# Optimization experiments

Measured on AMD Instinct MI355X. Metric: run time of the kernel, lower is better.

## Reference

```python
import jax, jax.numpy as jnp
import numpy as np
from jax.scipy.linalg import solve_triangular

N, S, G, D = 2048, 64, 1, 512


def setup_inputs() -> dict:
    key = jax.random.key(0)
    k1, k2, k3, k4 = jax.random.split(key, 4)
    x = jax.random.normal(k1, (N, D), jnp.float32)
    mu = jax.random.uniform(k2, (S, G, D), jnp.float32) - 0.5  # torch.rand(...) - 0.5
    omega = jax.random.normal(k3, (S, G), jnp.float32)
    # original init sets sigma_p = eye; perturb so m = A^T A has distinct eigenvalues
    sigma_p = jnp.eye(D, dtype=jnp.float32)[None, None] + 0.05 * jax.random.normal(k4, (S, G, D, D), jnp.float32)
    return {"x": x, "mu": mu, "omega": omega, "sigma_p": sigma_p}


def reference(x, mu, omega, sigma_p):
    d = x.shape[-1]
    # m = sigma_p^T @ sigma_p  (symmetric PSD), per class/component
    m = jnp.einsum('sgki,sgkj->sgij', sigma_p, sigma_p)  # (S,G,D,D)
    # torch: sigma = m + 0.01 * diag_embed(eig(m).eigenvalues.real) * eye(d)
    # m is symmetric PSD -> eigenvalues are real; eigvalsh is the batched symmetric form
    eigvals = jnp.linalg.eigvalsh(m)  # (S,G,D)
    sigma = m + 0.01 * eigvals[..., None] * jnp.eye(d, dtype=m.dtype)  # adds diag(eigvals)
    _ = jax.nn.softmax(omega, -1)  # computed in original forward but unused in output
    mu0 = mu[:, 0]        # (S,D)   only component 0 is used
    sig0 = sigma[:, 0]    # (S,D,D)
    # MultivariateNormal.log_prob via Cholesky, batched over classes and samples
    L = jnp.linalg.cholesky(sig0)               # (S,D,D)
    diff = x[None, :, :] - mu0[:, None, :]      # (S,N,D)
    z = solve_triangular(L, diff.swapaxes(-1, -2), lower=True)  # (S,D,N)
    maha = jnp.sum(z * z, axis=1)               # (S,N)
    logdet = 2.0 * jnp.sum(jnp.log(jnp.diagonal(L, axis1=-2, axis2=-1)), axis=-1)  # (S,)
    logp = -0.5 * (maha + logdet[:, None] + d * jnp.log(jnp.asarray(2.0 * np.pi, m.dtype)))
    return logp.T  # (N,S)
```

## Files before the change

### kernel.cpp

```cpp
#include <hip/hip_runtime.h>

#define D 512
#define TW 16

__device__ __forceinline__ float waveSum(float v) {
#pragma unroll
    for (int m = 32; m > 0; m >>= 1) v += __shfl_xor(v, m, 64);
    return v;
}
__device__ __forceinline__ float waveMin(float v) {
#pragma unroll
    for (int m = 32; m > 0; m >>= 1) v = fminf(v, __shfl_xor(v, m, 64));
    return v;
}
__device__ __forceinline__ float waveMax(float v) {
#pragma unroll
    for (int m = 32; m > 0; m >>= 1) v = fmaxf(v, __shfl_xor(v, m, 64));
    return v;
}

__global__ __launch_bounds__(256) void xpose_kernel(const float* __restrict__ x,
                                                    float* __restrict__ xT) {
    __shared__ float t[64][65];
    const int bx = blockIdx.x * 64;
    const int by = blockIdx.y * 64;
    const int tid = threadIdx.x;
    const int lx = tid & 63, lq = tid >> 6;
#pragma unroll
    for (int r = 0; r < 64; r += 4)
        t[r + lq][lx] = x[(size_t)(bx + r + lq) * D + by + lx];
    __syncthreads();
#pragma unroll
    for (int r = 0; r < 64; r += 4)
        xT[(size_t)(by + r + lq) * 2048 + bx + lx] = t[lx][r + lq];
}

__global__ __launch_bounds__(256) void syrk_kernel(const float* __restrict__ sp,
                                                   float* __restrict__ M) {
    const int s = blockIdx.y;
    const int I = blockIdx.x >> 3, J = blockIdx.x & 7;
    const int tx = threadIdx.x & 15, ty = threadIdx.x >> 4;
    const float* __restrict__ A = sp + (size_t)s * D * D;
    __shared__ __align__(16) float As[64 * 68];
    __shared__ __align__(16) float Bs[64 * 68];
    float acc[4][4];
#pragma unroll
    for (int r = 0; r < 4; r++)
#pragma unroll
        for (int q = 0; q < 4; q++) acc[r][q] = 0.f;

    for (int k0 = 0; k0 < D; k0 += 64) {
        for (int e = threadIdx.x; e < 4096; e += 256) {
            const int col = e & 63, kr = e >> 6;
            As[kr * 68 + col] = A[(size_t)(k0 + kr) * D + I * 64 + col];
            Bs[kr * 68 + col] = A[(size_t)(k0 + kr) * D + J * 64 + col];
        }
        __syncthreads();
#pragma unroll 4
        for (int k = 0; k < 64; k++) {
            const float4 a = *(const float4*)&As[k * 68 + 4 * ty];
            const float4 b = *(const float4*)&Bs[k * 68 + 4 * tx];
            const float av[4] = {a.x, a.y, a.z, a.w};
            const float bv[4] = {b.x, b.y, b.z, b.w};
#pragma unroll
            for (int r = 0; r < 4; r++)
#pragma unroll
                for (int q = 0; q < 4; q++) acc[r][q] += av[r] * bv[q];
        }
        __syncthreads();
    }
#pragma unroll
    for (int r = 0; r < 4; r++) {
        float4 v4;
        v4.x = acc[r][0]; v4.y = acc[r][1]; v4.z = acc[r][2]; v4.w = acc[r][3];
        const size_t off = (size_t)s * D * D + (size_t)(I * 64 + 4 * ty + r) * D + J * 64 + 4 * tx;
        *(float4*)(M + off) = v4;
    }
}

__global__ __launch_bounds__(1024) void latrd_panel(float* __restrict__ T,
                                                    float* __restrict__ Vt,
                                                    float* __restrict__ Wt,
                                                    float* __restrict__ dvec,
                                                    float* __restrict__ evec,
                                                    int ps, int jmax) {
    const int s = blockIdx.x;
    float* __restrict__ Ts = T + (size_t)s * D * D;
    float* __restrict__ Vg = Vt + (size_t)s * 32 * D;
    float* __restrict__ Wg = Wt + (size_t)s * 32 * D;
    const int tid = threadIdx.x, lane = tid & 63, wid = tid >> 6;
    const int l4 = lane & 15, quad = lane >> 4;
    extern __shared__ float sm[];
    float* __restrict__ Vs = sm;
    float* __restrict__ Ws = sm + 16896;
    float* __restrict__ vb = sm + 33792;
    float* __restrict__ pf = sm + 34304;
    float* __restrict__ c1 = sm + 34816;
    float* __restrict__ c2 = sm + 34848;
    float* __restrict__ red = sm + 34880;
    float* __restrict__ sca = sm + 34896;

    for (int i = tid; i < 34304; i += 1024) sm[i] = 0.f;
    __syncthreads();

    float rk = (tid < D) ? Ts[(size_t)ps * D + tid] : 0.f;

    for (int j = 0; j < jmax; j++) {
        const int k = ps + j, sup = k + 1;
        float val = 0.f;
        if (tid < D && tid > k) {
            float corr = 0.f;
#pragma unroll 4
            for (int t = 0; t < j; t++)
                corr += Vs[tid * 33 + t] * Ws[k * 33 + t]
                      + Ws[tid * 33 + t] * Vs[k * 33 + t];
            val = rk - corr;
            vb[tid] = val;
            if (tid == sup) sca[3] = val;
        } else if (tid == k) {
            float dc = 0.f;
            for (int t = 0; t < j; t++) dc += Vs[k * 33 + t] * Ws[k * 33 + t];
            dvec[s * D + k] = rk - 2.f * dc;
            vb[k] = 0.f;
        }
        float xp = (tid < D && tid > sup) ? val * val : 0.f;
        xp = waveSum(xp);
        if (lane == 0) red[wid] = xp;
        __syncthreads();

        float xn2 = 0.f;
#pragma unroll
        for (int q = 0; q < TW; q++) xn2 += red[q];
        const float a0 = sca[3];
        const int skip = (xn2 <= 0.f);
        float beta = 0.f, v0 = 0.f, alpha = a0;
        if (!skip) {
            const float an = sqrtf(a0 * a0 + xn2);
            alpha = (a0 >= 0.f) ? -an : an;
            v0 = a0 - alpha;
            beta = 2.f / (v0 * v0 + xn2);
        }
        if (tid == sup) {
            evec[s * D + k] = skip ? a0 : alpha;
            if (!skip) vb[sup] = v0;
        }
        if (!skip) {
            const int t = tid >> 5, r = tid & 31;
            float a1 = 0.f, a2 = 0.f;
            for (int i = sup + 1 + r; i < D; i += 32) {
                const float v = vb[i];
                a1 += Ws[i * 33 + t] * v;
                a2 += Vs[i * 33 + t] * v;
            }
#pragma unroll
            for (int m = 16; m > 0; m >>= 1) {
                a1 += __shfl_xor(a1, m, 64);
                a2 += __shfl_xor(a2, m, 64);
            }
            if (r == 0) {
                c1[t] = a1 + Ws[sup * 33 + t] * v0;
                c2[t] = a2 + Vs[sup * 33 + t] * v0;
            }
        }
        __syncthreads();
        if (skip) {
            if (tid < D && tid >= sup) { Vg[j * D + tid] = 0.f; Wg[j * D + tid] = 0.f; }
            if (tid < D && k + 1 < D) rk = Ts[(size_t)(k + 1) * D + tid];
            __syncthreads();
            continue;
        }

        const int w0 = sup & ~63;
        float pvw = 0.f;
        for (int i = sup + (wid * 4 + quad); i < D; i += 64) {
            const float* __restrict__ row = Ts + (size_t)i * D;
            float4 a4 = {0.f, 0.f, 0.f, 0.f};
            for (int c = w0 + 4 * l4; c < D; c += 64) {
                const float4 a = *(const float4*)&row[c];
                const float4 b = *(const float4*)&vb[c];
                a4.x += a.x * b.x; a4.y += a.y * b.y;
                a4.z += a.z * b.z; a4.w += a.w * b.w;
            }
            float t1 = (a4.x + a4.y) + (a4.z + a4.w);
            t1 -= Vs[i * 33 + l4] * c1[l4] + Vs[i * 33 + l4 + 16] * c1[l4 + 16]
                + Ws[i * 33 + l4] * c2[l4] + Ws[i * 33 + l4 + 16] * c2[l4 + 16];
#pragma unroll
            for (int m = 1; m < 16; m <<= 1) t1 += __shfl_xor(t1, m, 64);
            const float p = beta * t1;
            if (l4 == 0) pf[i] = p;
            pvw += p * vb[i];
        }
        pvw += __shfl_xor(pvw, 16, 64);
        pvw += __shfl_xor(pvw, 32, 64);
        if (lane == 0) red[wid] = pvw;
        __syncthreads();

        float pv = 0.f;
#pragma unroll
        for (int q = 0; q < TW; q++) pv += red[q];
        const float cc = 0.5f * beta * pv;
        if (tid < D) {
            if (tid >= sup) {
                const float v = vb[tid];
                const float w = pf[tid] - cc * v;
                Vs[tid * 33 + j] = v;
                Ws[tid * 33 + j] = w;
                Vg[j * D + tid] = v;
                Wg[j * D + tid] = w;
            }
            if (k + 1 < D) rk = Ts[(size_t)(k + 1) * D + tid];
        }
        __syncthreads();
    }
    if (ps + jmax == D - 2 && tid == 0) {
        const int k1 = D - 2, k2 = D - 1;
        float dc = 0.f, ec = 0.f, dc2 = 0.f;
        for (int t = 0; t < jmax; t++) {
            dc  += Vs[k1 * 33 + t] * Ws[k1 * 33 + t];
            ec  += Vs[k1 * 33 + t] * Ws[k2 * 33 + t]
                 + Ws[k1 * 33 + t] * Vs[k2 * 33 + t];
            dc2 += Vs[k2 * 33 + t] * Ws[k2 * 33 + t];
        }
        dvec[s * D + k1] = Ts[(size_t)k1 * D + k1] - 2.f * dc;
        evec[s * D + k1] = Ts[(size_t)k1 * D + k2] - ec;
        dvec[s * D + k2] = Ts[(size_t)k2 * D + k2] - 2.f * dc2;
        evec[s * D + k2] = 0.f;
    }
}

__global__ __launch_bounds__(256) void latrd_update(float* __restrict__ T,
                                                    const float* __restrict__ Vt,
                                                    const float* __restrict__ Wt,
                                                    int r0) {
    const int s = blockIdx.z;
    const int i0 = r0 + 64 * blockIdx.y;
    const int j0 = r0 + 64 * blockIdx.x;
    float* __restrict__ Ts = T + (size_t)s * D * D;
    const float* __restrict__ Vg = Vt + (size_t)s * 32 * D;
    const float* __restrict__ Wg = Wt + (size_t)s * 32 * D;
    __shared__ __align__(16) float Vi[32 * 68], Wi[32 * 68], Vj[32 * 68], Wj[32 * 68];
    const int tid = threadIdx.x, tx = tid & 15, ty = tid >> 4;
    const float4 z4 = {0.f, 0.f, 0.f, 0.f};
    for (int e = tid; e < 512; e += 256) {
        const int t = e >> 4, c4 = (e & 15) * 4;
        const int gi = i0 + c4, gj = j0 + c4;
        *(float4*)&Vi[t * 68 + c4] = (gi < D) ? *(const float4*)&Vg[t * D + gi] : z4;
        *(float4*)&Wi[t * 68 + c4] = (gi < D) ? *(const float4*)&Wg[t * D + gi] : z4;
        *(float4*)&Vj[t * 68 + c4] = (gj < D) ? *(const float4*)&Vg[t * D + gj] : z4;
        *(float4*)&Wj[t * 68 + c4] = (gj < D) ? *(const float4*)&Wg[t * D + gj] : z4;
    }
    __syncthreads();
    float acc[4][4] = {{0.f}};
#pragma unroll 4
    for (int t = 0; t < 32; t++) {
        const float4 va = *(const float4*)&Vi[t * 68 + 4 * ty];
        const float4 wa = *(const float4*)&Wi[t * 68 + 4 * ty];
        const float4 vc = *(const float4*)&Vj[t * 68 + 4 * tx];
        const float4 wc = *(const float4*)&Wj[t * 68 + 4 * tx];
        const float av[4] = {va.x, va.y, va.z, va.w};
        const float aw[4] = {wa.x, wa.y, wa.z, wa.w};
        const float bv[4] = {vc.x, vc.y, vc.z, vc.w};
        const float bw[4] = {wc.x, wc.y, wc.z, wc.w};
#pragma unroll
        for (int r = 0; r < 4; r++)
#pragma unroll
            for (int q = 0; q < 4; q++) acc[r][q] += av[r] * bw[q] + aw[r] * bv[q];
    }
    const int gj = j0 + 4 * tx;
    if (gj >= D) return;
#pragma unroll
    for (int r = 0; r < 4; r++) {
        const int gi = i0 + 4 * ty + r;
        if (gi >= D) continue;
        float4 c = *(float4*)&Ts[(size_t)gi * D + gj];
        c.x -= acc[r][0]; c.y -= acc[r][1]; c.z -= acc[r][2]; c.w -= acc[r][3];
        *(float4*)&Ts[(size_t)gi * D + gj] = c;
    }
}

__global__ __launch_bounds__(512) void bisect_kernel(const float* __restrict__ dvec,
                                                     const float* __restrict__ evec,
                                                     float* __restrict__ lam) {
    const int s = blockIdx.x, tid = threadIdx.x;
    const int lane = tid & 63, wid = tid >> 6;
    __shared__ float d[D], e2[D], ea[D];
    __shared__ float red[8];
    __shared__ float sh_lo, sh_hi;
    {
        const float dv = dvec[s * D + tid];
        const float ev = evec[s * D + tid];
        d[tid] = dv; ea[tid] = fabsf(ev); e2[tid] = ev * ev;
    }
    __syncthreads();
    const float rad = ea[tid] + ((tid > 0) ? ea[tid - 1] : 0.f);
    float lo = waveMin(d[tid] - rad);
    float hi = waveMax(d[tid] + rad);
    if (lane == 0) red[wid] = lo;
    __syncthreads();
    if (tid == 0) {
        float t = red[0];
        for (int q = 1; q < 8; q++) t = fminf(t, red[q]);
        sh_lo = t - 1e-3f * fmaxf(fabsf(t), 1.f);
    }
    __syncthreads();
    if (lane == 0) red[wid] = hi;
    __syncthreads();
    if (tid == 0) {
        float t = red[0];
        for (int q = 1; q < 8; q++) t = fmaxf(t, red[q]);
        sh_hi = t + 1e-3f * fmaxf(fabsf(t), 1.f);
    }
    __syncthreads();
    float a = sh_lo, b = sh_hi;
    const int j1 = tid + 1;
    for (int it = 0; it < 36; it++) {
        const float mid = 0.5f * (a + b);
        int cnt = 0;
        float q = d[0] - mid;
        cnt += (q < 0.f);
        for (int i = 1; i < D; i++) {
            float den = q;
            const float ad = fabsf(den);
            den = (ad < 1e-26f) ? ((den < 0.f) ? -1e-26f : 1e-26f) : den;
            q = d[i] - mid - e2[i - 1] / den;
            cnt += (q < 0.f);
        }
        if (cnt >= j1) b = mid; else a = mid;
    }
    lam[s * D + tid] = 0.5f * (a + b);
}

__global__ __launch_bounds__(256) void chol_panel(float* __restrict__ M,
                                                  const float* __restrict__ lam,
                                                  float* __restrict__ logdet,
                                                  float* __restrict__ Lp,
                                                  int j0, int first) {
    const int s = blockIdx.x;
    float* __restrict__ Ms = M + (size_t)s * D * D;
    float* __restrict__ Lps = Lp + (size_t)s * 32 * D;
    const int tid = threadIdx.x, lane = tid & 63, wid = tid >> 6;
    extern __shared__ float smc[];
    float* __restrict__ P = smc;
    const int Wd = D - j0;
    for (int e = tid; e < 32 * D; e += 256) {
        const int t = e >> 9, i = e & 511;
        if (i >= j0) {
            const int il = i - j0;
            float v = Ms[(size_t)(j0 + t) * D + i];
            if (il == t) v += 0.01f * lam[s * D + j0 + t];
            P[t * 520 + il] = v;
        }
    }
    __syncthreads();
    float lacc = 0.f;
    for (int jl = 0; jl < 32; jl++) {
        const float pd = P[jl * 520 + jl];
        const float inv = 1.f / sqrtf(pd);
        if (tid == 0) { lacc += 0.5f * logf(pd); P[jl * 520 + jl] = sqrtf(pd); }
        for (int il = jl + 1 + tid; il < Wd; il += 256) P[jl * 520 + il] *= inv;
        __syncthreads();
        for (int kk = jl + 1 + wid; kk < 32; kk += 4) {
            const float f = P[jl * 520 + kk];
            for (int il = kk + lane; il < Wd; il += 64) P[kk * 520 + il] -= f * P[jl * 520 + il];
        }
        __syncthreads();
    }
    if (tid == 0) logdet[s] = (first ? 0.f : logdet[s]) + 2.f * lacc;
    for (int e = tid; e < 32 * D; e += 256) {
        const int t = e >> 9, i = e & 511;
        const int il = i - j0;
        if (il >= t) Ms[(size_t)(j0 + t) * D + i] = P[t * 520 + il];
        if (i >= j0 + 32) Lps[(size_t)t * D + i] = P[t * 520 + il];
    }
}

__global__ __launch_bounds__(256) void chol_update(float* __restrict__ M,
                                                   const float* __restrict__ Lp,
                                                   int r0) {
    if (blockIdx.x < blockIdx.y) return;
    const int s = blockIdx.z;
    const int i0 = r0 + 64 * blockIdx.y;
    const int j0 = r0 + 64 * blockIdx.x;
    float* __restrict__ Ms = M + (size_t)s * D * D;
    const float* __restrict__ Lps = Lp + (size_t)s * 32 * D;
    __shared__ __align__(16) float Li[32 * 68], Lj[32 * 68];
    const int tid = threadIdx.x, tx = tid & 15, ty = tid >> 4;
    const float4 z4 = {0.f, 0.f, 0.f, 0.f};
    for (int e = tid; e < 512; e += 256) {
        const int t = e >> 4, c4 = (e & 15) * 4;
        const int gi = i0 + c4, gj = j0 + c4;
        *(float4*)&Li[t * 68 + c4] = (gi < D) ? *(const float4*)&Lps[(size_t)t * D + gi] : z4;
        *(float4*)&Lj[t * 68 + c4] = (gj < D) ? *(const float4*)&Lps[(size_t)t * D + gj] : z4;
    }
    __syncthreads();
    float acc[4][4] = {{0.f}};
#pragma unroll 4
    for (int t = 0; t < 32; t++) {
        const float4 a = *(const float4*)&Li[t * 68 + 4 * ty];
        const float4 b = *(const float4*)&Lj[t * 68 + 4 * tx];
        const float av[4] = {a.x, a.y, a.z, a.w};
        const float bv[4] = {b.x, b.y, b.z, b.w};
#pragma unroll
        for (int r = 0; r < 4; r++)
#pragma unroll
            for (int q = 0; q < 4; q++) acc[r][q] += av[r] * bv[q];
    }
    const int gj = j0 + 4 * tx;
    if (gj >= D) return;
#pragma unroll
    for (int r = 0; r < 4; r++) {
        const int gi = i0 + 4 * ty + r;
        if (gi >= D) continue;
        float4 c = *(float4*)&Ms[(size_t)gi * D + gj];
        c.x -= acc[r][0]; c.y -= acc[r][1]; c.z -= acc[r][2]; c.w -= acc[r][3];
        *(float4*)&Ms[(size_t)gi * D + gj] = c;
    }
}

__global__ __launch_bounds__(64) void invdiag_kernel(const float* __restrict__ M,
                                                     float* __restrict__ invDT) {
    const int b = blockIdx.x, s = b >> 3, I = b & 7;
    const int c = threadIdx.x;
    __shared__ float Lsh[64 * 65];
    __shared__ float xsh[64 * 65];
    const float* __restrict__ Ms = M + (size_t)s * D * D;
    for (int e = c; e < 4096; e += 64) {
        const int i = e & 63, k = e >> 6;
        Lsh[i * 65 + k] = Ms[(size_t)(I * 64 + k) * D + I * 64 + i];
    }
    for (int i = 0; i < 64; i++) xsh[c * 65 + i] = (i == c) ? 1.f : 0.f;
    __syncthreads();
    for (int i = 0; i < 64; i++) {
        float t = xsh[c * 65 + i];
        for (int k = 0; k < i; k++) t -= Lsh[i * 65 + k] * xsh[c * 65 + k];
        xsh[c * 65 + i] = t / Lsh[i * 65 + i];
    }
    float* __restrict__ outp = invDT + (size_t)b * 4096 + c * 64;
    for (int i = 0; i < 64; i++) outp[i] = xsh[c * 65 + i];
}

__global__ __launch_bounds__(256) void trsm_kernel(const float* __restrict__ M,
                                                   const float* __restrict__ invDT,
                                                   const float* __restrict__ xT,
                                                   const float* __restrict__ mu,
                                                   const float* __restrict__ logdet,
                                                   float* __restrict__ out) {
    extern __shared__ float smem[];
    float* __restrict__ Z = smem;
    float* __restrict__ U = smem + 512 * 33;
    const int s = blockIdx.y;
    const int n0 = blockIdx.x * 32;
    const int tid = threadIdx.x;
    const int tx = tid & 15, ty = tid >> 4;
    const float* __restrict__ Ms = M + (size_t)s * D * D;
    const float* __restrict__ mus = mu + s * D;

    for (int I = 0; I < 8; I++) {
        float acc[4][2];
#pragma unroll
        for (int r = 0; r < 4; r++) {
            const int irow = I * 64 + 4 * ty + r;
            const float m0 = mus[irow];
            const float2 xv = *(const float2*)&xT[(size_t)irow * 2048 + n0 + 2 * tx];
            acc[r][0] = xv.x - m0;
            acc[r][1] = xv.y - m0;
        }
        for (int J = 0; J < I; J++) {
#pragma unroll
            for (int h = 0; h < 2; h++) {
                __syncthreads();
                for (int e = tid; e < 512; e += 256) {
                    const int i4 = (e & 15) * 4, kk = e >> 4;
                    *(float4*)&U[kk * 68 + i4] =
                        *(const float4*)&Ms[(size_t)(J * 64 + 32 * h + kk) * D + I * 64 + i4];
                }
                __syncthreads();
#pragma unroll 8
                for (int kk = 0; kk < 32; kk++) {
                    const float4 a = *(const float4*)&U[kk * 68 + 4 * ty];
                    const float2 b = *(const float2*)&Z[(J * 64 + 32 * h + kk) * 33 + 2 * tx];
                    const float av[4] = {a.x, a.y, a.z, a.w};
#pragma unroll
                    for (int r = 0; r < 4; r++) {
                        acc[r][0] -= av[r] * b.x;
                        acc[r][1] -= av[r] * b.y;
                    }
                }
            }
        }
        __syncthreads();
#pragma unroll
        for (int r = 0; r < 4; r++) {
            float2 v2; v2.x = acc[r][0]; v2.y = acc[r][1];
            *(float2*)&U[(4 * ty + r) * 34 + 2 * tx] = v2;
        }
        __syncthreads();
        {
            float z[4][2] = {{0.f}};
            const float* __restrict__ iD = invDT + (size_t)(s * 8 + I) * 4096;
#pragma unroll 8
            for (int kk = 0; kk < 64; kk++) {
                const float4 a = *(const float4*)&iD[kk * 64 + 4 * ty];
                const float2 b = *(const float2*)&U[kk * 34 + 2 * tx];
                const float av[4] = {a.x, a.y, a.z, a.w};
#pragma unroll
                for (int r = 0; r < 4; r++) {
                    z[r][0] += av[r] * b.x;
                    z[r][1] += av[r] * b.y;
                }
            }
#pragma unroll
            for (int r = 0; r < 4; r++) {
                float2 v2; v2.x = z[r][0]; v2.y = z[r][1];
                *(float2*)&Z[(I * 64 + 4 * ty + r) * 33 + 2 * tx] = v2;
            }
        }
    }
    __syncthreads();
    {
        const int c = tid & 31, part = tid >> 5;
        float sum = 0.f;
        for (int i = part * 64; i < part * 64 + 64; i++) {
            const float z = Z[i * 33 + c];
            sum += z * z;
        }
        U[part * 32 + c] = sum;
    }
    __syncthreads();
    if (tid < 32) {
        float mah = 0.f;
#pragma unroll
        for (int p = 0; p < 8; p++) mah += U[p * 32 + tid];
        out[(size_t)(n0 + tid) * 64 + s] = -0.5f * (mah + logdet[s] + 940.993058f);
    }
}

extern "C" void kernel_launch(void* const* d_in, const int* in_sizes, int n_in,
                              void* d_out, int out_size, void* d_ws, size_t ws_size,
                              hipStream_t stream) {
    const float* x  = (const float*)d_in[0];
    const float* mu = (const float*)d_in[1];
    const float* sp = (const float*)d_in[3];
    float* out = (float*)d_out;

    float* wsf  = (float*)d_ws;
    float* MT   = wsf;
    float* dvec = wsf + (size_t)16777216;
    float* evec = dvec + 32768;
    float* lamv = evec + 32768;
    float* logd = lamv + 32768;
    float* Vt   = logd + 64;
    float* Wt   = Vt + (size_t)1048576;
    float* xT   = Wt + (size_t)1048576;
    float* Lp   = Vt;
    float* invDT = Vt;

    xpose_kernel<<<dim3(32, 8), dim3(256), 0, stream>>>(x, xT);
    syrk_kernel<<<dim3(64, 64), dim3(256), 0, stream>>>(sp, MT);

    const size_t plds = (size_t)34900 * sizeof(float);
    for (int p = 0; p < 16; p++) {
        const int ps = 32 * p;
        const int jmax = (p == 15) ? 30 : 32;
        latrd_panel<<<dim3(64), dim3(1024), plds, stream>>>(MT, Vt, Wt, dvec, evec, ps, jmax);
        if (p < 15) {
            const int r0 = ps + 32;
            const int nt = (D - r0 + 63) / 64;
            latrd_update<<<dim3(nt, nt, 64), dim3(256), 0, stream>>>(MT, Vt, Wt, r0);
        }
    }

    bisect_kernel<<<dim3(64), dim3(512), 0, stream>>>(dvec, evec, lamv);

    syrk_kernel<<<dim3(64, 64), dim3(256), 0, stream>>>(sp, MT);
    const size_t clds = (size_t)(32 * 520 + 4) * sizeof(float);
    for (int p = 0; p < 16; p++) {
        const int j0 = 32 * p;
        chol_panel<<<dim3(64), dim3(256), clds, stream>>>(MT, lamv, logd, Lp, j0, p == 0 ? 1 : 0);
        if (p < 15) {
            const int r0 = j0 + 32;
            const int nt = (D - r0 + 63) / 64;
            chol_update<<<dim3(nt, nt, 64), dim3(256), 0, stream>>>(MT, Lp, r0);
        }
    }

    invdiag_kernel<<<dim3(512), dim3(64), 0, stream>>>(MT, invDT);

    const size_t tlds = (size_t)(512 * 33 + 2176) * sizeof(float);
    trsm_kernel<<<dim3(64, 64), dim3(256), tlds, stream>>>(MT, invDT, xT, mu, logd, out);
}
```

Baseline: 12.00 ms.

## Replace blocked forward substitution with explicit triangular inverse then GEMM

The per-sample triangular solve, which walked block rows one after another, is replaced by building the full inverse of the Cholesky factor in place. Seven launches of a block-row inversion step form the off-diagonal inverse blocks. A dense lower-triangular GEMM then multiplies that inverse by (x - mu) and reduces the squared norms into the Mahalanobis term. This trades the serial dependency chain inside the solve for parallel GEMM work, at the cost of extra launches, an in-place overwrite of the factor, and possible numerical differences from explicit inversion.

New measurement: 11.14 ms. 1.08x faster.

```diff
diff --git a/kernel.cpp b/kernel.cpp
--- a/kernel.cpp
+++ b/kernel.cpp
@@ -439,98 +439,154 @@
     for (int i = 0; i < 64; i++) outp[i] = xsh[c * 65 + i];
 }
 
-__global__ __launch_bounds__(256) void trsm_kernel(const float* __restrict__ M,
+__global__ __launch_bounds__(256) void triinv_step(float* __restrict__ M,
                                                    const float* __restrict__ invDT,
-                                                   const float* __restrict__ xT,
-                                                   const float* __restrict__ mu,
-                                                   const float* __restrict__ logdet,
-                                                   float* __restrict__ out) {
-    extern __shared__ float smem[];
-    float* __restrict__ Z = smem;
-    float* __restrict__ U = smem + 512 * 33;
+                                                   int I) {
+    const int J = blockIdx.x, s = blockIdx.y;
+    float* __restrict__ Ms = M + (size_t)s * D * D;
+    __shared__ __align__(16) float Ls[64 * 68];
+    __shared__ __align__(16) float Bs[64 * 68];
+    __shared__ __align__(16) float Ss[64 * 68];
+    const int tid = threadIdx.x, tx = tid & 15, ty = tid >> 4;
+    float acc[4][4] = {{0.f}};
+    for (int K = J; K < I; K++) {
+        __syncthreads();
+        for (int e = tid; e < 4096; e += 256) {
+            const int k = e >> 6, r = e & 63;
+            Ls[k * 68 + r] = Ms[(size_t)(K * 64 + k) * D + I * 64 + r];
+        }
+        if (K == J) {
+            const float* __restrict__ dJ = invDT + ((size_t)s * 8 + J) * 4096;
+            for (int e = tid; e < 4096; e += 256) {
+                const int c = e >> 6, k = e & 63;
+                Bs[k * 68 + c] = dJ[c * 64 + k];
+            }
+        } else {
+            for (int e = tid; e < 4096; e += 256) {
+                const int k = e >> 6, c = e & 63;
+                Bs[k * 68 + c] = Ms[(size_t)(K * 64 + k) * D + J * 64 + c];
+            }
+        }
+        __syncthreads();
+#pragma unroll 4
+        for (int k = 0; k < 64; k++) {
+            const float4 a = *(const float4*)&Ls[k * 68 + 4 * ty];
+            const float4 b = *(const float4*)&Bs[k * 68 + 4 * tx];
+            const float av[4] = {a.x, a.y, a.z, a.w};
+            const float bv[4] = {b.x, b.y, b.z, b.w};
+#pragma unroll
+            for (int r = 0; r < 4; r++)
+#pragma unroll
+                for (int q = 0; q < 4; q++) acc[r][q] += av[r] * bv[q];
+        }
+    }
+    __syncthreads();
+#pragma unroll
+    for (int r = 0; r < 4; r++) {
+        float4 v4;
+        v4.x = acc[r][0]; v4.y = acc[r][1]; v4.z = acc[r][2]; v4.w = acc[r][3];
+        *(float4*)&Ss[(4 * ty + r) * 68 + 4 * tx] = v4;
+    }
+    {
+        const float* __restrict__ dI = invDT + ((size_t)s * 8 + I) * 4096;
+        for (int e = tid; e < 4096; e += 256) {
+            const int k = e >> 6, r = e & 63;
+            Ls[k * 68 + r] = dI[k * 64 + r];
+        }
+    }
+    __syncthreads();
+    float o[4][4] = {{0.f}};
+#pragma unroll 4
+    for (int k = 0; k < 64; k++) {
+        const float4 a = *(const float4*)&Ls[k * 68 + 4 * ty];
+        const float4 b = *(const float4*)&Ss[k * 68 + 4 * tx];
+        const float av[4] = {a.x, a.y, a.z, a.w};
+        const float bv[4] = {b.x, b.y, b.z, b.w};
+#pragma unroll
+        for (int r = 0; r < 4; r++)
+#pragma unroll
+            for (int q = 0; q < 4; q++) o[r][q] += av[r] * bv[q];
+    }
+#pragma unroll
+    for (int r = 0; r < 4; r++) {
+        float4 v4;
+        v4.x = -o[r][0]; v4.y = -o[r][1]; v4.z = -o[r][2]; v4.w = -o[r][3];
+        *(float4*)&Ms[(size_t)(I * 64 + 4 * ty + r) * D + J * 64 + 4 * tx] = v4;
+    }
+}
+
+__global__ __launch_bounds__(256) void gemm_maha(const float* __restrict__ M,
+                                                 const float* __restrict__ invDT,
+                                                 const float* __restrict__ xT,
+                                                 const float* __restrict__ mu,
+                                                 const float* __restrict__ logdet,
+                                                 float* __restrict__ out) {
     const int s = blockIdx.y;
-    const int n0 = blockIdx.x * 32;
-    const int tid = threadIdx.x;
-    const int tx = tid & 15, ty = tid >> 4;
+    const int n0 = blockIdx.x * 64;
+    const int tid = threadIdx.x, tx = tid & 15, ty = tid >> 4;
     const float* __restrict__ Ms = M + (size_t)s * D * D;
     const float* __restrict__ mus = mu + s * D;
-
-    for (int I = 0; I < 8; I++) {
-        float acc[4][2];
-#pragma unroll
-        for (int r = 0; r < 4; r++) {
-            const int irow = I * 64 + 4 * ty + r;
-            const float m0 = mus[irow];
-            const float2 xv = *(const float2*)&xT[(size_t)irow * 2048 + n0 + 2 * tx];
-            acc[r][0] = xv.x - m0;
-            acc[r][1] = xv.y - m0;
-        }
-        for (int J = 0; J < I; J++) {
-#pragma unroll
-            for (int h = 0; h < 2; h++) {
-                __syncthreads();
-                for (int e = tid; e < 512; e += 256) {
-                    const int i4 = (e & 15) * 4, kk = e >> 4;
-                    *(float4*)&U[kk * 68 + i4] =
-                        *(const float4*)&Ms[(size_t)(J * 64 + 32 * h + kk) * D + I * 64 + i4];
+    __shared__ __align__(16) float As[32 * 136];
+    __shared__ __align__(16) float Bs[32 * 68];
+    __shared__ float red[16 * 68];
+    float cs[4] = {0.f, 0.f, 0.f, 0.f};
+
+    for (int ci = 0; ci < 4; ci++) {
+        const int i0 = ci * 128;
+        float acc[8][4];
+#pragma unroll
+        for (int r = 0; r < 8; r++)
+#pragma unroll
+            for (int q = 0; q < 4; q++) acc[r][q] = 0.f;
+        const int nkc = (ci + 1) * 4;
+        for (int kc = 0; kc < nkc; kc++) {
+            const int k0 = kc * 32, kb = k0 >> 6;
+            __syncthreads();
+            for (int e = tid; e < 4096; e += 256) {
+                const int il = e >> 5, kk = e & 31;
+                const int ib = (i0 + il) >> 6;
+                As[kk * 136 + il] = (kb < ib) ? Ms[(size_t)(i0 + il) * D + k0 + kk] : 0.f;
+            }
+            if (kb >= 2 * ci) {
+                const float* __restrict__ dB = invDT + ((size_t)s * 8 + kb) * 4096
+                                             + (size_t)(k0 & 63) * 64;
+                const int ilb = (kb - 2 * ci) * 64;
+                for (int e = tid; e < 2048; e += 256) {
+                    const int ii = e & 63, kk = e >> 6;
+                    As[kk * 136 + ilb + ii] = dB[kk * 64 + ii];
                 }
-                __syncthreads();
+            }
+            for (int e = tid; e < 2048; e += 256) {
+                const int nn = e & 63, kk = e >> 6;
+                Bs[kk * 68 + nn] = xT[(size_t)(k0 + kk) * 2048 + n0 + nn] - mus[k0 + kk];
+            }
+            __syncthreads();
 #pragma unroll 8
-                for (int kk = 0; kk < 32; kk++) {
-                    const float4 a = *(const float4*)&U[kk * 68 + 4 * ty];
-                    const float2 b = *(const float2*)&Z[(J * 64 + 32 * h + kk) * 33 + 2 * tx];
-                    const float av[4] = {a.x, a.y, a.z, a.w};
-#pragma unroll
-                    for (int r = 0; r < 4; r++) {
-                        acc[r][0] -= av[r] * b.x;
-                        acc[r][1] -= av[r] * b.y;
-                    }
-                }
-            }
-        }
-        __syncthreads();
-#pragma unroll
-        for (int r = 0; r < 4; r++) {
-            float2 v2; v2.x = acc[r][0]; v2.y = acc[r][1];
-            *(float2*)&U[(4 * ty + r) * 34 + 2 * tx] = v2;
-        }
-        __syncthreads();
-        {
-            float z[4][2] = {{0.f}};
-            const float* __restrict__ iD = invDT + (size_t)(s * 8 + I) * 4096;
-#pragma unroll 8
-            for (int kk = 0; kk < 64; kk++) {
-                const float4 a = *(const float4*)&iD[kk * 64 + 4 * ty];
-                const float2 b = *(const float2*)&U[kk * 34 + 2 * tx];
-                const float av[4] = {a.x, a.y, a.z, a.w};
-#pragma unroll
-                for (int r = 0; r < 4; r++) {
-                    z[r][0] += av[r] * b.x;
-                    z[r][1] += av[r] * b.y;
-                }
-            }
-#pragma unroll
-            for (int r = 0; r < 4; r++) {
-                float2 v2; v2.x = z[r][0]; v2.y = z[r][1];
-                *(float2*)&Z[(I * 64 + 4 * ty + r) * 33 + 2 * tx] = v2;
-            }
-        }
-    }
-    __syncthreads();
-    {
-        const int c = tid & 31, part = tid >> 5;
-        float sum = 0.f;
-        for (int i = part * 64; i < part * 64 + 64; i++) {
-            const float z = Z[i * 33 + c];
-            sum += z * z;
-        }
-        U[part * 32 + c] = sum;
-    }
-    __syncthreads();
-    if (tid < 32) {
+            for (int kk = 0; kk < 32; kk++) {
+                const float4 a0 = *(const float4*)&As[kk * 136 + 8 * ty];
+                const float4 a1 = *(const float4*)&As[kk * 136 + 8 * ty + 4];
+                const float4 b  = *(const float4*)&Bs[kk * 68 + 4 * tx];
+                const float av[8] = {a0.x, a0.y, a0.z, a0.w, a1.x, a1.y, a1.z, a1.w};
+                const float bv[4] = {b.x, b.y, b.z, b.w};
+#pragma unroll
+                for (int r = 0; r < 8; r++)
+#pragma unroll
+                    for (int q = 0; q < 4; q++) acc[r][q] += av[r] * bv[q];
+            }
+        }
+#pragma unroll
+        for (int r = 0; r < 8; r++)
+#pragma unroll
+            for (int q = 0; q < 4; q++) cs[q] += acc[r][q] * acc[r][q];
+    }
+    __syncthreads();
+#pragma unroll
+    for (int q = 0; q < 4; q++) red[ty * 68 + 4 * tx + q] = cs[q];
+    __syncthreads();
+    if (tid < 64) {
         float mah = 0.f;
 #pragma unroll
-        for (int p = 0; p < 8; p++) mah += U[p * 32 + tid];
+        for (int t = 0; t < 16; t++) mah += red[t * 68 + tid];
         out[(size_t)(n0 + tid) * 64 + s] = -0.5f * (mah + logdet[s] + 940.993058f);
     }
 }
@@ -585,7 +641,8 @@
     }
 
     invdiag_kernel<<<dim3(512), dim3(64), 0, stream>>>(MT, invDT);
-
-    const size_t tlds = (size_t)(512 * 33 + 2176) * sizeof(float);
-    trsm_kernel<<<dim3(64, 64), dim3(256), tlds, stream>>>(MT, invDT, xT, mu, logd, out);
-}
+    for (int I = 1; I < 8; I++)
+        triinv_step<<<dim3(I, 64), dim3(256), 0, stream>>>(MT, invDT, I);
+
+    gemm_maha<<<dim3(32, 64), dim3(256), 0, stream>>>(MT, invDT, xT, mu, logd, out);
+}
```
